# Kernel optimization log

Hardware: AMD Instinct MI355X
Metric: run time of the kernel (lower is better)

Reference implementation:

```python
import jax, jax.numpy as jnp
import numpy as np

N_NODES = 200000
N_EDGES = 6400000
N_GRAPHS = 1024
N_EMB = 1032
D = 16


def _gcn_conv(x, W, b, src, dst, n):
    # PyG GCNConv: h = x W; symmetric norm with self-loops; aggregate onto target (dst)
    h = x @ W
    deg = jax.ops.segment_sum(jnp.ones_like(dst, dtype=h.dtype), dst, num_segments=n) + 1.0
    dis = jax.lax.rsqrt(deg)
    norm = dis[src] * dis[dst]                      # [E]
    agg = jax.ops.segment_sum(h[src] * norm[:, None], dst, num_segments=n)
    agg = agg + h * (dis * dis)[:, None]            # self-loop term
    return agg + b


def _protein_embed(ids, edge_index, batch_ids, emb, W1, b1, W2, b2):
    n = ids.shape[0]
    x = emb[ids]                                    # embedding lookup [N, D]
    src, dst = edge_index[0], edge_index[1]
    h = jax.nn.relu(_gcn_conv(x, W1, b1, src, dst, n))
    h = _gcn_conv(h, W2, b2, src, dst, n)
    # global_mean_pool over graphs
    sums = jax.ops.segment_sum(h, batch_ids, num_segments=N_GRAPHS)
    cnt = jax.ops.segment_sum(jnp.ones((n,), h.dtype), batch_ids, num_segments=N_GRAPHS)
    return sums / jnp.maximum(cnt, 1.0)[:, None]    # [B, D]


def setup_inputs() -> dict:
    key = jax.random.key(0)
    ks = jax.random.split(key, 10)
    emb = jax.random.normal(ks[0], (N_EMB, D), jnp.float32) * 0.1
    W1 = jax.random.normal(ks[1], (D, D), jnp.float32) * (1.0 / np.sqrt(D))
    W2 = jax.random.normal(ks[2], (D, D), jnp.float32) * (1.0 / np.sqrt(D))
    fcW = jax.random.normal(ks[3], (6, 2 * D), jnp.float32) * (1.0 / np.sqrt(2 * D))
    b1 = jnp.zeros((D,), jnp.float32)
    b2 = jnp.zeros((D,), jnp.float32)
    fcb = jnp.zeros((6,), jnp.float32)
    rx = jax.random.randint(ks[4], (N_NODES,), 0, N_EMB)
    r_edge_index = jax.random.randint(ks[5], (2, N_EDGES), 0, N_NODES)
    r_batch = jnp.sort(jax.random.randint(ks[6], (N_NODES,), 0, N_GRAPHS))
    lx = jax.random.randint(ks[7], (N_NODES,), 0, N_EMB)
    l_edge_index = jax.random.randint(ks[8], (2, N_EDGES), 0, N_NODES)
    l_batch = jnp.sort(jax.random.randint(ks[9], (N_NODES,), 0, N_GRAPHS))
    return {"emb": emb, "W1": W1, "b1": b1, "W2": W2, "b2": b2, "fcW": fcW, "fcb": fcb,
            "rx": rx, "r_edge_index": r_edge_index, "r_batch": r_batch,
            "lx": lx, "l_edge_index": l_edge_index, "l_batch": l_batch}


def reference(emb, W1, b1, W2, b2, fcW, fcb, rx, r_edge_index, r_batch, lx, l_edge_index, l_batch):
    r = _protein_embed(rx, r_edge_index, r_batch, emb, W1, b1, W2, b2)
    l = _protein_embed(lx, l_edge_index, l_batch, emb, W1, b1, W2, b2)
    h = jnp.concatenate([r, l], axis=1)             # [B, 2D]
    out = h @ fcW.T + fcb                           # [B, 6]
    return out[:, :3], out[:, 3:]
```

## Files before the change

kernel.cpp:

```cpp
#include <hip/hip_runtime.h>
#include <hip/hip_bf16.h>

#define N_NODES 200000
#define N_GRAPHS 1024
#define D 16
#define NEDGE 6400000

#define BNODES 256
#define NBUK 782
#define NCH 640
#define ECHUNK 10000
#define CAP 9216
#define GHALF 6250

__global__ __launch_bounds__(1024) void pA(
        const int* __restrict__ srcR, const int* __restrict__ dstR,
        const int* __restrict__ srcL, const int* __restrict__ dstL,
        unsigned int* __restrict__ slabR, unsigned int* __restrict__ slabL,
        int* __restrict__ gcurR, int* __restrict__ gcurL) {
    const int* src = blockIdx.y ? srcL : srcR;
    const int* dst = blockIdx.y ? dstL : dstR;
    unsigned int* slab = blockIdx.y ? slabL : slabR;
    int* gcur = blockIdx.y ? gcurL : gcurR;

    __shared__ unsigned int stage[ECHUNK];
    __shared__ unsigned short stageB[ECHUNK];
    __shared__ int lh[NBUK];
    __shared__ int lcur[NBUK];
    __shared__ int wsum[16];
    int t = threadIdx.x;
    int wave = t >> 6, lane = t & 63;
    int base = blockIdx.x * ECHUNK;

    for (int k = t; k < NBUK; k += 1024) lh[k] = 0;
    __syncthreads();
    for (int e = t; e < ECHUNK; e += 1024)
        atomicAdd(&lh[((unsigned int)dst[base + e]) >> 8], 1);
    __syncthreads();

    int v = (t < NBUK) ? lh[t] : 0;
    int x = v;
#pragma unroll
    for (int d0 = 1; d0 < 64; d0 <<= 1) {
        int y = __shfl_up(x, d0, 64);
        if (lane >= d0) x += y;
    }
    if (lane == 63) wsum[wave] = x;
    __syncthreads();
    if (wave == 0 && lane < 16) {
        int s = wsum[lane];
#pragma unroll
        for (int d0 = 1; d0 < 16; d0 <<= 1) {
            int y = __shfl_up(s, d0, 64);
            if (lane >= d0) s += y;
        }
        wsum[lane] = s;
    }
    __syncthreads();
    int excl = x - v + (wave ? wsum[wave - 1] : 0);
    if (t < NBUK) lcur[t] = excl;
    __syncthreads();
    if (t < NBUK) {
        int gb = v ? atomicAdd(&gcur[t], v) : 0;
        lh[t] = gb - excl;
    }
    __syncthreads();

    for (int e = t; e < ECHUNK; e += 1024) {
        int d = dst[base + e];
        int s = src[base + e];
        int buk = ((unsigned int)d) >> 8;
        int pos = atomicAdd(&lcur[buk], 1);
        stage[pos] = ((unsigned int)(d & 255) << 18) | (unsigned int)s;
        stageB[pos] = (unsigned short)buk;
    }
    __syncthreads();
    for (int e = t; e < ECHUNK; e += 1024) {
        int k = stageB[e];
        int off = lh[k] + e;
        slab[(size_t)k * CAP + off] = stage[e];
    }
}

__global__ __launch_bounds__(512) void pB2(
        unsigned int* __restrict__ slabR, unsigned int* __restrict__ slabL,
        const int* __restrict__ gcurR, const int* __restrict__ gcurL,
        const int* __restrict__ idsR, const int* __restrict__ idsL,
        const float* __restrict__ emb, const float* __restrict__ W1,
        int2* __restrict__ metaR, int2* __restrict__ metaL,
        float* __restrict__ disR, float* __restrict__ disL,
        __hip_bfloat16* __restrict__ hs1R, __hip_bfloat16* __restrict__ hs1L) {
    int y = blockIdx.y;
    unsigned int* slab = y ? slabL : slabR;
    const int* gcur = y ? gcurL : gcurR;
    const int* ids = y ? idsL : idsR;
    int2* meta = y ? metaL : metaR;
    float* dis = y ? disL : disR;
    __hip_bfloat16* hs1 = y ? hs1L : hs1R;

    __shared__ unsigned int sout[CAP];
    __shared__ int hcnt[BNODES], hoff[BNODES], hcur[BNODES];
    __shared__ float sW[D][D];
    __shared__ int wtot[4];
    int t = threadIdx.x;
    int b = blockIdx.x;
    if (t < 256) { sW[t >> 4][t & 15] = W1[t]; hcnt[t] = 0; }
    int cnt = gcur[b]; if (cnt > CAP) cnt = CAP;
    unsigned int* sl = slab + (size_t)b * CAP;
    __syncthreads();

    for (int i = t; i < cnt; i += 512)
        atomicAdd(&hcnt[sl[i] >> 18], 1);
    __syncthreads();

    int lane = t & 63, wave = t >> 6;
    int v2 = (t < 256) ? hcnt[t] : 0;
    int x2 = v2;
#pragma unroll
    for (int d0 = 1; d0 < 64; d0 <<= 1) {
        int yy = __shfl_up(x2, d0, 64);
        if (lane >= d0) x2 += yy;
    }
    if (t < 256 && lane == 63) wtot[wave] = x2;
    __syncthreads();
    if (t < 256) {
        int pre2 = 0;
        for (int w2 = 0; w2 < wave; w2++) pre2 += wtot[w2];
        int ex = x2 - v2 + pre2;
        hoff[t] = ex;
        hcur[t] = ex;
    }
    __syncthreads();

    for (int i = t; i < cnt; i += 512) {
        unsigned int r = sl[i];
        int pp = atomicAdd(&hcur[r >> 18], 1);
        if (pp < CAP) sout[pp] = r & 0x3FFFFu;
    }
    __syncthreads();

    for (int i = t; i < cnt; i += 512) sl[i] = sout[i];

    int tt = t >> 1, hf = t & 1;
    int node = (b << 8) + tt;
    if (node < N_NODES) {
        int hc = hcnt[tt];
        float di = rsqrtf((float)hc + 1.0f);
        int gb = b * CAP;
        if (hf == 0) {
            meta[node] = make_int2(gb + hoff[tt], gb + hoff[tt] + hc);
            dis[node] = di;
        }
        const float4* er = (const float4*)(emb + (size_t)ids[node] * D);
        float4 e0 = er[0], e1 = er[1], e2 = er[2], e3 = er[3];
        float ex_[D] = {e0.x, e0.y, e0.z, e0.w, e1.x, e1.y, e1.z, e1.w,
                        e2.x, e2.y, e2.z, e2.w, e3.x, e3.y, e3.z, e3.w};
        int j0 = hf * 8;
        float o[8];
#pragma unroll
        for (int jj = 0; jj < 8; jj++) {
            float a = 0.f;
#pragma unroll
            for (int k = 0; k < D; k++) a += ex_[k] * sW[k][j0 + jj];
            o[jj] = a * di;
        }
        uint4 ov;
        __hip_bfloat162* q = (__hip_bfloat162*)&ov;
#pragma unroll
        for (int jj = 0; jj < 4; jj++)
            q[jj] = __float22bfloat162_rn(make_float2(o[2 * jj], o[2 * jj + 1]));
        *(uint4*)(hs1 + (size_t)node * D + j0) = ov;
    }
}

__global__ __launch_bounds__(256) void g1_kernel(
        const int2* __restrict__ metaR, const int2* __restrict__ metaL,
        const unsigned int* __restrict__ csrR, const unsigned int* __restrict__ csrL,
        const __hip_bfloat16* __restrict__ hs1R, const __hip_bfloat16* __restrict__ hs1L,
        const float* __restrict__ disR, const float* __restrict__ disL,
        const float* __restrict__ b1, const float* __restrict__ W2,
        __hip_bfloat16* __restrict__ hs2R, __hip_bfloat16* __restrict__ hs2L) {
    int half = (blockIdx.x >= GHALF);
    int bx = blockIdx.x - (half ? GHALF : 0);
    const int2* meta = half ? metaL : metaR;
    const unsigned int* csr = half ? csrL : csrR;
    const __hip_bfloat16* hs1 = half ? hs1L : hs1R;
    const float* dis = half ? disL : disR;
    __hip_bfloat16* hs2 = half ? hs2L : hs2R;

    __shared__ float sW[D][D];
    __shared__ float sx[32][D + 1];
    int t = threadIdx.x;
    int jp = t & 7, g = t >> 3;
    sW[t >> 4][t & 15] = W2[t];
    int i = (bx << 5) + g;
    int2 be = meta[i];
    float2 acc = __bfloat1622float2(
        *(const __hip_bfloat162*)(hs1 + (size_t)i * D + 2 * jp));
    int e = be.x, end = be.y;
    for (; e + 8 <= end; e += 8) {
        int my = (int)csr[e + jp];
#pragma unroll
        for (int n = 0; n < 8; n++) {
            int s = __shfl(my, n, 8);
            float2 f = __bfloat1622float2(
                *(const __hip_bfloat162*)(hs1 + (size_t)s * D + 2 * jp));
            acc.x += f.x; acc.y += f.y;
        }
    }
    for (; e < end; e++) {
        int s = csr[e];
        float2 f = __bfloat1622float2(
            *(const __hip_bfloat162*)(hs1 + (size_t)s * D + 2 * jp));
        acc.x += f.x; acc.y += f.y;
    }
    float di = dis[i];
    sx[g][2 * jp]     = fmaxf(acc.x * di + b1[2 * jp], 0.f);
    sx[g][2 * jp + 1] = fmaxf(acc.y * di + b1[2 * jp + 1], 0.f);
    __syncthreads();
    float a0 = 0.f, a1 = 0.f;
#pragma unroll
    for (int k = 0; k < D; k++) {
        float xv = sx[g][k];
        a0 += xv * sW[k][2 * jp];
        a1 += xv * sW[k][2 * jp + 1];
    }
    *(__hip_bfloat162*)(hs2 + (size_t)i * D + 2 * jp) =
        __float22bfloat162_rn(make_float2(a0 * di, a1 * di));
}

__global__ __launch_bounds__(256) void g2_kernel(
        const int2* __restrict__ metaR, const int2* __restrict__ metaL,
        const unsigned int* __restrict__ csrR, const unsigned int* __restrict__ csrL,
        const __hip_bfloat16* __restrict__ hs2R, const __hip_bfloat16* __restrict__ hs2L,
        const float* __restrict__ disR, const float* __restrict__ disL,
        const float* __restrict__ b2,
        const int* __restrict__ batR, const int* __restrict__ batL,
        float* __restrict__ sumsR, float* __restrict__ sumsL,
        float* __restrict__ cntR, float* __restrict__ cntL) {
    int half = (blockIdx.x >= GHALF);
    int bx = blockIdx.x - (half ? GHALF : 0);
    const int2* meta = half ? metaL : metaR;
    const unsigned int* csr = half ? csrL : csrR;
    const __hip_bfloat16* hs2 = half ? hs2L : hs2R;
    const float* dis = half ? disL : disR;
    const int* batch = half ? batL : batR;
    float* sums = half ? sumsL : sumsR;
    float* cnt = half ? cntL : cntR;

    __shared__ float sv[32][D + 1];
    __shared__ int sb[32];
    int t = threadIdx.x;
    int jp = t & 7, g = t >> 3;
    int i = (bx << 5) + g;
    int2 be = meta[i];
    float2 acc = __bfloat1622float2(
        *(const __hip_bfloat162*)(hs2 + (size_t)i * D + 2 * jp));
    int e = be.x, end = be.y;
    for (; e + 8 <= end; e += 8) {
        int my = (int)csr[e + jp];
#pragma unroll
        for (int n = 0; n < 8; n++) {
            int s = __shfl(my, n, 8);
            float2 f = __bfloat1622float2(
                *(const __hip_bfloat162*)(hs2 + (size_t)s * D + 2 * jp));
            acc.x += f.x; acc.y += f.y;
        }
    }
    for (; e < end; e++) {
        int s = csr[e];
        float2 f = __bfloat1622float2(
            *(const __hip_bfloat162*)(hs2 + (size_t)s * D + 2 * jp));
        acc.x += f.x; acc.y += f.y;
    }
    float di = dis[i];
    int bi = batch[i];
    sv[g][2 * jp]     = acc.x * di + b2[2 * jp];
    sv[g][2 * jp + 1] = acc.y * di + b2[2 * jp + 1];
    if (jp == 0) sb[g] = bi;
    __syncthreads();
    bool runend = (g == 31) || (sb[g + 1] != bi);
    if (runend) {
        float s0 = 0.f, s1 = 0.f;
        int gg = g;
        while (gg >= 0 && sb[gg] == bi) { s0 += sv[gg][2 * jp]; s1 += sv[gg][2 * jp + 1]; gg--; }
        atomicAdd(&sums[bi * D + 2 * jp], s0);
        atomicAdd(&sums[bi * D + 2 * jp + 1], s1);
        if (jp == 0) atomicAdd(&cnt[bi], (float)(g - gg));
    }
}

__global__ void final_kernel(const float* __restrict__ rs, const float* __restrict__ rc,
                             const float* __restrict__ ls, const float* __restrict__ lc,
                             const float* __restrict__ fcW, const float* __restrict__ fcb,
                             float* __restrict__ out) {
    int b = blockIdx.x * blockDim.x + threadIdx.x;
    if (b >= N_GRAPHS) return;
    float hc[2 * D];
    float rn = fmaxf(rc[b], 1.f), ln = fmaxf(lc[b], 1.f);
#pragma unroll
    for (int j = 0; j < D; j++) {
        hc[j]     = rs[b * D + j] / rn;
        hc[D + j] = ls[b * D + j] / ln;
    }
#pragma unroll
    for (int c = 0; c < 6; c++) {
        float acc = fcb[c];
#pragma unroll
        for (int j = 0; j < 2 * D; j++) acc += hc[j] * fcW[c * 2 * D + j];
        if (c < 3) out[b * 3 + c] = acc;
        else       out[N_GRAPHS * 3 + b * 3 + (c - 3)] = acc;
    }
}

extern "C" void kernel_launch(void* const* d_in, const int* in_sizes, int n_in,
                              void* d_out, int out_size, void* d_ws, size_t ws_size,
                              hipStream_t stream) {
    const float* emb = (const float*)d_in[0];
    const float* W1  = (const float*)d_in[1];
    const float* b1  = (const float*)d_in[2];
    const float* W2  = (const float*)d_in[3];
    const float* b2  = (const float*)d_in[4];
    const float* fcW = (const float*)d_in[5];
    const float* fcb = (const float*)d_in[6];
    const int* rx = (const int*)d_in[7];
    const int* re = (const int*)d_in[8];
    const int* rb = (const int*)d_in[9];
    const int* lx = (const int*)d_in[10];
    const int* le = (const int*)d_in[11];
    const int* lb = (const int*)d_in[12];
    float* out = (float*)d_out;

    char* w = (char*)d_ws;
    unsigned int* slabR = (unsigned int*)w;    w += (size_t)NBUK * CAP * 4;
    unsigned int* slabL = (unsigned int*)w;    w += (size_t)NBUK * CAP * 4;
    __hip_bfloat16* hs1R = (__hip_bfloat16*)w; w += (size_t)N_NODES * D * 2;
    __hip_bfloat16* hs1L = (__hip_bfloat16*)w; w += (size_t)N_NODES * D * 2;
    __hip_bfloat16* hs2R = (__hip_bfloat16*)w; w += (size_t)N_NODES * D * 2;
    __hip_bfloat16* hs2L = (__hip_bfloat16*)w; w += (size_t)N_NODES * D * 2;
    int2* metaR = (int2*)w;                    w += (size_t)N_NODES * 8;
    int2* metaL = (int2*)w;                    w += (size_t)N_NODES * 8;
    float* disR = (float*)w;                   w += (size_t)N_NODES * 4;
    float* disL = (float*)w;                   w += (size_t)N_NODES * 4;
    char* zbase = w;
    int* gcurR = (int*)w;                      w += (size_t)NBUK * 4;
    int* gcurL = (int*)w;                      w += (size_t)NBUK * 4;
    float* sums0 = (float*)w;                  w += (size_t)N_GRAPHS * D * 4;
    float* cnt0  = (float*)w;                  w += (size_t)N_GRAPHS * 4;
    float* sums1 = (float*)w;                  w += (size_t)N_GRAPHS * D * 4;
    float* cnt1  = (float*)w;                  w += (size_t)N_GRAPHS * 4;
    size_t zsize = (size_t)(w - zbase);

    const int* srcR = re;  const int* dstR = re + NEDGE;
    const int* srcL = le;  const int* dstL = le + NEDGE;

    hipMemsetAsync(zbase, 0, zsize, stream);

    pA<<<dim3(NCH, 2), 1024, 0, stream>>>(srcR, dstR, srcL, dstL,
                                          slabR, slabL, gcurR, gcurL);
    pB2<<<dim3(NBUK, 2), 512, 0, stream>>>(slabR, slabL, gcurR, gcurL,
                                           rx, lx, emb, W1,
                                           metaR, metaL, disR, disL, hs1R, hs1L);

    g1_kernel<<<2 * GHALF, 256, 0, stream>>>(metaR, metaL, slabR, slabL,
                                             hs1R, hs1L, disR, disL, b1, W2, hs2R, hs2L);
    g2_kernel<<<2 * GHALF, 256, 0, stream>>>(metaR, metaL, slabR, slabL,
                                             hs2R, hs2L, disR, disL, b2, rb, lb,
                                             sums0, sums1, cnt0, cnt1);
    final_kernel<<<(N_GRAPHS + 255) / 256, 256, 0, stream>>>(
        sums0, cnt0, sums1, cnt1, fcW, fcb, out);
}
```

Baseline: 513.3 us.

## Privatize LDS bucket histograms per wave group to cut atomic contention

Splits the shared-memory histograms and cursors in the edge-bucketing kernel pA and the per-bucket sort kernel pB2 into four sub-histograms, one per group of waves. Each sub-histogram's cursor starts at an offset derived from the earlier groups, so the placement stays consistent. This reduces LDS atomic contention on hot bins. It also shrinks the pA edge chunk from 10000 to 8000 and raises the chunk count to 800, which costs some extra setup and scan work per block and slightly more global atomics on the bucket counters.

```diff
diff --git a/kernel.cpp b/kernel.cpp
--- a/kernel.cpp
+++ b/kernel.cpp
@@ -8,10 +8,11 @@
 
 #define BNODES 256
 #define NBUK 782
-#define NCH 640
-#define ECHUNK 10000
+#define NCH 800
+#define ECHUNK 8000
 #define CAP 9216
 #define GHALF 6250
+#define NSUB 4
 
 __global__ __launch_bounds__(1024) void pA(
         const int* __restrict__ srcR, const int* __restrict__ dstR,
@@ -25,20 +26,25 @@
 
     __shared__ unsigned int stage[ECHUNK];
     __shared__ unsigned short stageB[ECHUNK];
-    __shared__ int lh[NBUK];
-    __shared__ int lcur[NBUK];
+    __shared__ int lh[NSUB][NBUK];
+    __shared__ int lcur[NSUB][NBUK];
     __shared__ int wsum[16];
     int t = threadIdx.x;
     int wave = t >> 6, lane = t & 63;
+    int sub = wave >> 2;
     int base = blockIdx.x * ECHUNK;
 
-    for (int k = t; k < NBUK; k += 1024) lh[k] = 0;
+    for (int k = t; k < NSUB * NBUK; k += 1024) ((int*)lh)[k] = 0;
     __syncthreads();
     for (int e = t; e < ECHUNK; e += 1024)
-        atomicAdd(&lh[((unsigned int)dst[base + e]) >> 8], 1);
-    __syncthreads();
-
-    int v = (t < NBUK) ? lh[t] : 0;
+        atomicAdd(&lh[sub][((unsigned int)dst[base + e]) >> 8], 1);
+    __syncthreads();
+
+    int l0 = 0, l1 = 0, l2 = 0, l3 = 0, v = 0;
+    if (t < NBUK) {
+        l0 = lh[0][t]; l1 = lh[1][t]; l2 = lh[2][t]; l3 = lh[3][t];
+        v = l0 + l1 + l2 + l3;
+    }
     int x = v;
 #pragma unroll
     for (int d0 = 1; d0 < 64; d0 <<= 1) {
@@ -58,11 +64,13 @@
     }
     __syncthreads();
     int excl = x - v + (wave ? wsum[wave - 1] : 0);
-    if (t < NBUK) lcur[t] = excl;
-    __syncthreads();
     if (t < NBUK) {
+        lcur[0][t] = excl;
+        lcur[1][t] = excl + l0;
+        lcur[2][t] = excl + l0 + l1;
+        lcur[3][t] = excl + l0 + l1 + l2;
         int gb = v ? atomicAdd(&gcur[t], v) : 0;
-        lh[t] = gb - excl;
+        lh[0][t] = gb - excl;
     }
     __syncthreads();
 
@@ -70,15 +78,14 @@
         int d = dst[base + e];
         int s = src[base + e];
         int buk = ((unsigned int)d) >> 8;
-        int pos = atomicAdd(&lcur[buk], 1);
+        int pos = atomicAdd(&lcur[sub][buk], 1);
         stage[pos] = ((unsigned int)(d & 255) << 18) | (unsigned int)s;
         stageB[pos] = (unsigned short)buk;
     }
     __syncthreads();
     for (int e = t; e < ECHUNK; e += 1024) {
         int k = stageB[e];
-        int off = lh[k] + e;
-        slab[(size_t)k * CAP + off] = stage[e];
+        slab[(size_t)k * CAP + lh[0][k] + e] = stage[e];
     }
 }
 
@@ -99,22 +106,31 @@
     __hip_bfloat16* hs1 = y ? hs1L : hs1R;
 
     __shared__ unsigned int sout[CAP];
-    __shared__ int hcnt[BNODES], hoff[BNODES], hcur[BNODES];
+    __shared__ int hcnt[NSUB][BNODES];
+    __shared__ int hcur[NSUB][BNODES];
+    __shared__ int hoff[BNODES];
+    __shared__ int htot[BNODES];
     __shared__ float sW[D][D];
     __shared__ int wtot[4];
     int t = threadIdx.x;
+    int lane = t & 63, wave = t >> 6;
+    int sub = wave >> 1;
     int b = blockIdx.x;
-    if (t < 256) { sW[t >> 4][t & 15] = W1[t]; hcnt[t] = 0; }
+    if (t < 256) sW[t >> 4][t & 15] = W1[t];
+    for (int k = t; k < NSUB * BNODES; k += 512) ((int*)hcnt)[k] = 0;
     int cnt = gcur[b]; if (cnt > CAP) cnt = CAP;
     unsigned int* sl = slab + (size_t)b * CAP;
     __syncthreads();
 
     for (int i = t; i < cnt; i += 512)
-        atomicAdd(&hcnt[sl[i] >> 18], 1);
-    __syncthreads();
-
-    int lane = t & 63, wave = t >> 6;
-    int v2 = (t < 256) ? hcnt[t] : 0;
+        atomicAdd(&hcnt[sub][sl[i] >> 18], 1);
+    __syncthreads();
+
+    int c0 = 0, c1 = 0, c2 = 0, c3 = 0, v2 = 0;
+    if (t < 256) {
+        c0 = hcnt[0][t]; c1 = hcnt[1][t]; c2 = hcnt[2][t]; c3 = hcnt[3][t];
+        v2 = c0 + c1 + c2 + c3;
+    }
     int x2 = v2;
 #pragma unroll
     for (int d0 = 1; d0 < 64; d0 <<= 1) {
@@ -128,13 +144,17 @@
         for (int w2 = 0; w2 < wave; w2++) pre2 += wtot[w2];
         int ex = x2 - v2 + pre2;
         hoff[t] = ex;
-        hcur[t] = ex;
+        htot[t] = v2;
+        hcur[0][t] = ex;
+        hcur[1][t] = ex + c0;
+        hcur[2][t] = ex + c0 + c1;
+        hcur[3][t] = ex + c0 + c1 + c2;
     }
     __syncthreads();
 
     for (int i = t; i < cnt; i += 512) {
         unsigned int r = sl[i];
-        int pp = atomicAdd(&hcur[r >> 18], 1);
+        int pp = atomicAdd(&hcur[sub][r >> 18], 1);
         if (pp < CAP) sout[pp] = r & 0x3FFFFu;
     }
     __syncthreads();
@@ -144,7 +164,7 @@
     int tt = t >> 1, hf = t & 1;
     int node = (b << 8) + tt;
     if (node < N_NODES) {
-        int hc = hcnt[tt];
+        int hc = htot[tt];
         float di = rsqrtf((float)hc + 1.0f);
         int gb = b * CAP;
         if (hf == 0) {
```

Result: no change. 519.5 us (+1.2%).
